# Kernel tuning notes

Measured on AMD Instinct MI355X. Metric: run time of the kernel, lower is better.

## Reference

```python
import jax, jax.numpy as jnp
import numpy as np

H = 16          # num heads
DH = 64         # head dim
D = H * DH      # hidden = 1024


def setup_inputs() -> dict:
    key = jax.random.key(0)
    ks = jax.random.split(key, 9)
    s = 1.0 / np.sqrt(D)
    return {
        "hidden_states": jax.random.normal(ks[0], (4, 2048, D), dtype=jnp.float32),
        "Wq": jax.random.normal(ks[1], (D, D), dtype=jnp.float32) * s,
        "bq": jax.random.normal(ks[2], (D,), dtype=jnp.float32) * 0.02,
        "Wk": jax.random.normal(ks[3], (D, D), dtype=jnp.float32) * s,
        "bk": jax.random.normal(ks[4], (D,), dtype=jnp.float32) * 0.02,
        "Wv": jax.random.normal(ks[5], (D, D), dtype=jnp.float32) * s,
        "bv": jax.random.normal(ks[6], (D,), dtype=jnp.float32) * 0.02,
        "Wo": jax.random.normal(ks[7], (D, D), dtype=jnp.float32) * s,
        "bo": jax.random.normal(ks[8], (D,), dtype=jnp.float32) * 0.02,
    }


def _split_heads(x):  # [B,S,D] -> [B,H,S,DH]
    B, S, _ = x.shape
    return x.reshape(B, S, H, DH).transpose(0, 2, 1, 3)


def reference(hidden_states, Wq, bq, Wk, bk, Wv, bv, Wo, bo):
    # torch Linear: y = x @ W.T + b  (W stored as [out, in])
    q = _split_heads(jnp.einsum('bsd,ed->bse', hidden_states, Wq) + bq)
    k = _split_heads(jnp.einsum('bsd,ed->bse', hidden_states, Wk) + bk)
    v = _split_heads(jnp.einsum('bsd,ed->bse', hidden_states, Wv) + bv)
    scores = jnp.einsum('bhqd,bhkd->bhqk', q, k) / np.sqrt(DH)
    probs = jax.nn.softmax(scores, axis=-1)  # fused softmax+matmul in original
    ctx = jnp.einsum('bhqk,bhkd->bhqd', probs, v)
    B, _, S, _ = ctx.shape
    ctx = ctx.transpose(0, 2, 1, 3).reshape(B, S, D)
    out = jnp.einsum('bsd,ed->bse', ctx, Wo) + bo
    return out  # weights are None (vis=False); dropout rate asserted 0
```

## Files before the change

### kernel.cpp

```cpp
#include <hip/hip_runtime.h>


typedef __bf16 bf16;
typedef __bf16 bf16x8 __attribute__((ext_vector_type(8)));
typedef __bf16 bf16x4 __attribute__((ext_vector_type(4)));
typedef short  short4v __attribute__((ext_vector_type(4)));
typedef float  floatx4 __attribute__((ext_vector_type(4)));

#define NB   4
#define SEQ  2048
#define NH   16
#define DH   64
#define DIM  1024
#define MTOT (NB * SEQ)

#define CEXP 0.18033688f

__device__ __forceinline__ floatx4 zero4() {
    floatx4 z; z[0] = 0.f; z[1] = 0.f; z[2] = 0.f; z[3] = 0.f; return z;
}

__device__ __forceinline__ void load_lds16(const bf16* g, bf16* l) {
    __builtin_amdgcn_global_load_lds(
        (__attribute__((address_space(1))) void*)g,
        (__attribute__((address_space(3))) void*)l,
        16, 0, 0);
}

__device__ __forceinline__ short4v pk4(float a, float b, float c, float d) {
    bf16x4 t; t[0] = (bf16)a; t[1] = (bf16)b; t[2] = (bf16)c; t[3] = (bf16)d;
    return __builtin_bit_cast(short4v, t);
}

__global__ __launch_bounds__(256) void cvt_all(const float* __restrict__ X,
                                               const float* __restrict__ w0,
                                               const float* __restrict__ w1,
                                               const float* __restrict__ w2,
                                               const float* __restrict__ w3,
                                               bf16* __restrict__ Xb,
                                               bf16* __restrict__ Wb) {
    const size_t MD = (size_t)MTOT * DIM;
    const size_t DD = (size_t)DIM * DIM;
    size_t i = ((size_t)blockIdx.x * 256 + threadIdx.x) * 4;
    float4 f; bf16* dst;
    if (i < MD) {
        f = *(const float4*)(X + i);
        dst = Xb + i;
    } else {
        size_t off = i - MD;
        int w = (int)(off >> 20);
        size_t wi = off & (DD - 1);
        const float* ws = (w == 0) ? w0 : (w == 1) ? w1 : (w == 2) ? w2 : w3;
        f = *(const float4*)(ws + wi);
        dst = Wb + off;
    }
    bf16x4 o;
    o[0] = (bf16)f.x; o[1] = (bf16)f.y; o[2] = (bf16)f.z; o[3] = (bf16)f.w;
    *(bf16x4*)dst = o;
}

__global__ __launch_bounds__(256) void gemm_qkv(const bf16* __restrict__ A,
                                                const bf16* __restrict__ W,
                                                const float* __restrict__ bq,
                                                const float* __restrict__ bk,
                                                const float* __restrict__ bv,
                                                bf16* __restrict__ Qo,
                                                bf16* __restrict__ Ko,
                                                bf16* __restrict__ Vt) {
    __shared__ __align__(16) bf16 As[128 * 32];
    __shared__ __align__(16) bf16 Bs[128 * 32];
    __shared__ __align__(16) bf16 Ts[64 * 136];

    const int tid  = threadIdx.x;
    const int wave = tid >> 6, lane = tid & 63;
    const int quad = lane >> 4, l16 = lane & 15;
    const int sel = blockIdx.x >> 3;
    const int nt  = blockIdx.x & 7;
    const int m0 = blockIdx.y * 128, n0 = nt * 128;
    const int wm = (wave & 1) * 64, wn = (wave >> 1) * 64;
    const bf16* Wsel = W + (size_t)(sel * DIM + n0) * DIM;
    const float* bias = (sel == 0) ? bq : (sel == 1) ? bk : bv;
    const float scale = (sel == 0) ? CEXP : 1.0f;

    floatx4 acc[4][4];
#pragma unroll
    for (int mi = 0; mi < 4; mi++)
#pragma unroll
        for (int ni = 0; ni < 4; ni++) acc[mi][ni] = zero4();

    for (int k0 = 0; k0 < DIM; k0 += 32) {
        __syncthreads();
#pragma unroll
        for (int i = 0; i < 2; i++) {
            const int cb = wave * 128 + i * 64;
            const int c  = cb + lane;
            const int row = c >> 2;
            const int kc  = (c & 3) * 8;
            load_lds16(A + (size_t)(m0 + row) * DIM + k0 + kc, &As[cb * 8]);
            load_lds16(Wsel + (size_t)row * DIM + k0 + kc, &Bs[cb * 8]);
        }
        __syncthreads();

        bf16x8 af[4], bfr[4];
#pragma unroll
        for (int mi = 0; mi < 4; mi++)
            af[mi] = *(const bf16x8*)&As[(wm + mi * 16 + l16) * 32 + quad * 8];
#pragma unroll
        for (int ni = 0; ni < 4; ni++)
            bfr[ni] = *(const bf16x8*)&Bs[(wn + ni * 16 + l16) * 32 + quad * 8];
#pragma unroll
        for (int mi = 0; mi < 4; mi++)
#pragma unroll
            for (int ni = 0; ni < 4; ni++)
                acc[mi][ni] = __builtin_amdgcn_mfma_f32_16x16x32_bf16(
                    af[mi], bfr[ni], acc[mi][ni], 0, 0, 0);
    }

    if (sel < 2) {
        bf16* C = (sel == 0) ? Qo : Ko;
#pragma unroll
        for (int mi = 0; mi < 4; mi++) {
            const int rbase = m0 + wm + mi * 16 + quad * 4;
#pragma unroll
            for (int ni = 0; ni < 4; ni++) {
                const int col = n0 + wn + ni * 16 + l16;
                const float bval = bias[col];
#pragma unroll
                for (int i = 0; i < 4; i++)
                    C[(size_t)(rbase + i) * DIM + col] =
                        (bf16)((acc[mi][ni][i] + bval) * scale);
            }
        }
    } else {
        const int b  = blockIdx.y >> 4;
        const int s0 = (blockIdx.y & 15) * 128;
#pragma unroll
        for (int r = 0; r < 2; r++) {
            __syncthreads();
            if ((wave >> 1) == r) {
#pragma unroll
                for (int mi = 0; mi < 4; mi++) {
                    const int m_l = wm + mi * 16 + quad * 4;
#pragma unroll
                    for (int ni = 0; ni < 4; ni++) {
                        const int n_loc = ni * 16 + l16;
                        const float bval = bias[n0 + 64 * r + n_loc];
#pragma unroll
                        for (int i = 0; i < 4; i++)
                            Ts[n_loc * 136 + m_l + i] = (bf16)(acc[mi][ni][i] + bval);
                    }
                }
            }
            __syncthreads();
            const int hh = 2 * nt + r;
            bf16* obase = Vt + ((size_t)(b * NH + hh) * DH) * SEQ + s0;
#pragma unroll
            for (int p = 0; p < 4; p++) {
                const int chunk = p * 256 + tid;
                const int row = chunk >> 4, c0 = (chunk & 15) * 8;
                bf16x8 v = *(const bf16x8*)&Ts[row * 136 + c0];
                *(bf16x8*)(obase + (size_t)row * SEQ + c0) = v;
            }
        }
    }
}

__global__ __launch_bounds__(256) void gemm_out(const bf16* __restrict__ A,
                                                const bf16* __restrict__ W,
                                                const float* __restrict__ bias,
                                                float* __restrict__ C) {
    __shared__ __align__(16) bf16 As[128 * 32];
    __shared__ __align__(16) bf16 Bs[128 * 32];

    const int tid  = threadIdx.x;
    const int wave = tid >> 6, lane = tid & 63;
    const int quad = lane >> 4, l16 = lane & 15;
    const int m0 = blockIdx.y * 128, n0 = blockIdx.x * 128;
    const int wm = (wave & 1) * 64, wn = (wave >> 1) * 64;

    floatx4 acc[4][4];
#pragma unroll
    for (int mi = 0; mi < 4; mi++)
#pragma unroll
        for (int ni = 0; ni < 4; ni++) acc[mi][ni] = zero4();

    for (int k0 = 0; k0 < DIM; k0 += 32) {
        __syncthreads();
#pragma unroll
        for (int i = 0; i < 2; i++) {
            const int cb = wave * 128 + i * 64;
            const int c  = cb + lane;
            const int row = c >> 2;
            const int kc  = (c & 3) * 8;
            load_lds16(A + (size_t)(m0 + row) * DIM + k0 + kc, &As[cb * 8]);
            load_lds16(W + (size_t)(n0 + row) * DIM + k0 + kc, &Bs[cb * 8]);
        }
        __syncthreads();

        bf16x8 af[4], bfr[4];
#pragma unroll
        for (int mi = 0; mi < 4; mi++)
            af[mi] = *(const bf16x8*)&As[(wm + mi * 16 + l16) * 32 + quad * 8];
#pragma unroll
        for (int ni = 0; ni < 4; ni++)
            bfr[ni] = *(const bf16x8*)&Bs[(wn + ni * 16 + l16) * 32 + quad * 8];
#pragma unroll
        for (int mi = 0; mi < 4; mi++)
#pragma unroll
            for (int ni = 0; ni < 4; ni++)
                acc[mi][ni] = __builtin_amdgcn_mfma_f32_16x16x32_bf16(
                    af[mi], bfr[ni], acc[mi][ni], 0, 0, 0);
    }

#pragma unroll
    for (int mi = 0; mi < 4; mi++) {
        const int rbase = m0 + wm + mi * 16 + quad * 4;
#pragma unroll
        for (int ni = 0; ni < 4; ni++) {
            const int col = n0 + wn + ni * 16 + l16;
            const float bval = bias[col];
#pragma unroll
            for (int i = 0; i < 4; i++)
                C[(size_t)(rbase + i) * DIM + col] = acc[mi][ni][i] + bval;
        }
    }
}

__global__ __launch_bounds__(256, 6) void attn_kernel(const bf16* __restrict__ Q,
                                                      const bf16* __restrict__ K,
                                                      const bf16* __restrict__ Vt,
                                                      bf16* __restrict__ Ctx) {
    __shared__ __align__(16) bf16 Ks[2][64 * 64];
    __shared__ __align__(16) bf16 Vs[2][64 * 64];

    const int tid  = threadIdx.x;
    const int wave = tid >> 6, lane = tid & 63;
    const int quad = lane >> 4, l16 = lane & 15;
    const int bh = blockIdx.x >> 5;
    const int qb = blockIdx.x & 31;
    const int b  = bh >> 4, h = bh & 15;

    const size_t base_bh = (size_t)b * SEQ * DIM + (size_t)h * DH;
    const size_t base_v  = (size_t)bh * DH * SEQ;
    const bf16* Kg = K + base_bh;
    const bf16* Vg = Vt + base_v;
    const int qt = qb * 64 + wave * 16;

    const bf16* qp = Q + base_bh + (size_t)(qt + l16) * DIM + quad * 8;
    const bf16x8 aq0 = *(const bf16x8*)qp;
    const bf16x8 aq1 = *(const bf16x8*)(qp + 32);

    const int sc  = wave * 128 + lane;
    const int sr0 = sc >> 3,        sr1 = (sc + 64) >> 3;
    const int sc0 = (sc & 7) ^ (sr0 & 7), sc1 = ((sc + 64) & 7) ^ (sr1 & 7);
    const bf16* kga = Kg + (size_t)sr0 * DIM + sc0 * 8;
    const bf16* kgb = Kg + (size_t)sr1 * DIM + sc1 * 8;
    const bf16* vga = Vg + (size_t)sr0 * SEQ + sc0 * 8;
    const bf16* vgb = Vg + (size_t)sr1 * SEQ + sc1 * 8;

    int koa[4], kob[4], vo[4][4];
#pragma unroll
    for (int t = 0; t < 4; t++) {
        const int krow = t * 16 + l16;
        koa[t] = (krow * 8 + (quad ^ (krow & 7))) * 8;
        kob[t] = (krow * 8 + ((4 + quad) ^ (krow & 7))) * 8;
#pragma unroll
        for (int dt = 0; dt < 4; dt++) {
            const int d = dt * 16 + l16;
            vo[t][dt] = (d * 8 + ((t * 2 + (quad >> 1)) ^ (d & 7))) * 8
                        + (quad & 1) * 4;
        }
    }

    const short4v ones4 = pk4(1.f, 1.f, 1.f, 1.f);

    floatx4 acc[4], accl = zero4();
#pragma unroll
    for (int dt = 0; dt < 4; dt++) acc[dt] = zero4();

    load_lds16(kga, &Ks[0][(wave * 128) * 8]);
    load_lds16(kgb, &Ks[0][(wave * 128 + 64) * 8]);
    load_lds16(vga, &Vs[0][(wave * 128) * 8]);
    load_lds16(vgb, &Vs[0][(wave * 128 + 64) * 8]);

    for (int it = 0; it < SEQ / 64; it++) {
        __syncthreads();
        const int cur = it & 1;
        if (it + 1 < SEQ / 64) {
            const int nxt = cur ^ 1;
            const size_t kvn = (size_t)(it + 1) * 64;
            load_lds16(kga + kvn * DIM, &Ks[nxt][(wave * 128) * 8]);
            load_lds16(kgb + kvn * DIM, &Ks[nxt][(wave * 128 + 64) * 8]);
            load_lds16(vga + kvn, &Vs[nxt][(wave * 128) * 8]);
            load_lds16(vgb + kvn, &Vs[nxt][(wave * 128 + 64) * 8]);
        }

#pragma unroll
        for (int t = 0; t < 4; t++) {
            const bf16x8 kb0 = *(const bf16x8*)&Ks[cur][koa[t]];
            const bf16x8 kb1 = *(const bf16x8*)&Ks[cur][kob[t]];
            short4v vb[4];
#pragma unroll
            for (int dt = 0; dt < 4; dt++)
                vb[dt] = __builtin_bit_cast(short4v,
                    *(const bf16x4*)&Vs[cur][vo[t][dt]]);
            floatx4 z = zero4();
            z = __builtin_amdgcn_mfma_f32_16x16x32_bf16(kb0, aq0, z, 0, 0, 0);
            z = __builtin_amdgcn_mfma_f32_16x16x32_bf16(kb1, aq1, z, 0, 0, 0);
            const short4v p = pk4(__builtin_amdgcn_exp2f(z[0]),
                                  __builtin_amdgcn_exp2f(z[1]),
                                  __builtin_amdgcn_exp2f(z[2]),
                                  __builtin_amdgcn_exp2f(z[3]));
#pragma unroll
            for (int dt = 0; dt < 4; dt++)
                acc[dt] = __builtin_amdgcn_mfma_f32_16x16x16bf16_1k(
                    p, vb[dt], acc[dt], 0, 0, 0);
            accl = __builtin_amdgcn_mfma_f32_16x16x16bf16_1k(
                p, ones4, accl, 0, 0, 0);
        }
    }

    float inv[4];
#pragma unroll
    for (int i = 0; i < 4; i++) inv[i] = 1.0f / accl[i];
    bf16* cp = Ctx + base_bh + (size_t)(qt + quad * 4) * DIM + l16;
#pragma unroll
    for (int i = 0; i < 4; i++)
#pragma unroll
        for (int dt = 0; dt < 4; dt++)
            cp[(size_t)i * DIM + dt * 16] = (bf16)(acc[dt][i] * inv[i]);
}

extern "C" void kernel_launch(void* const* d_in, const int* in_sizes, int n_in,
                              void* d_out, int out_size, void* d_ws, size_t ws_size,
                              hipStream_t stream) {
    const float* X  = (const float*)d_in[0];
    const float* Wq = (const float*)d_in[1];
    const float* bq = (const float*)d_in[2];
    const float* Wk = (const float*)d_in[3];
    const float* bk = (const float*)d_in[4];
    const float* Wv = (const float*)d_in[5];
    const float* bv = (const float*)d_in[6];
    const float* Wo = (const float*)d_in[7];
    const float* bo = (const float*)d_in[8];
    float* out = (float*)d_out;

    const size_t MD = (size_t)MTOT * DIM;
    const size_t DD = (size_t)DIM * DIM;

    bf16* Xb  = (bf16*)d_ws;
    bf16* Qb  = Xb + MD;
    bf16* Kb  = Qb + MD;
    bf16* Vtb = Kb + MD;
    bf16* Wqb = Vtb + MD;
    bf16* Wob = Wqb + 3 * DD;
    if (ws_size < (MD * 4 + DD * 4) * sizeof(bf16)) return;

    cvt_all<<<(int)((MD + 4 * DD) / 4 / 256), 256, 0, stream>>>(
        X, Wq, Wk, Wv, Wo, Xb, Wqb);

    gemm_qkv<<<dim3(24, MTOT / 128), 256, 0, stream>>>(Xb, Wqb, bq, bk, bv,
                                                       Qb, Kb, Vtb);

    attn_kernel<<<NB * NH * (SEQ / 64), 256, 0, stream>>>(Qb, Kb, Vtb, Xb);

    gemm_out<<<dim3(8, MTOT / 128), 256, 0, stream>>>(Xb, Wob, bo, out);
}
```

Baseline: 312.1 us.

## Enlarge attention blocks to 128 queries and halve output GEMM M-tile

The attention kernel now runs 512-thread blocks covering 128 queries (8 waves), so each K/V tile staged in LDS is shared by twice as many queries and every thread issues one load per tile instead of two. The output projection GEMM switches to a 64x128 tile, doubling its grid to 1024 blocks to improve occupancy across CUs. The cost is fewer attention blocks (1024), higher register pressure under the 512-thread launch bound, and less reuse per block in the output GEMM.

```diff
diff --git a/kernel.cpp b/kernel.cpp
--- a/kernel.cpp
+++ b/kernel.cpp
@@ -169,43 +169,47 @@
                                                 const bf16* __restrict__ W,
                                                 const float* __restrict__ bias,
                                                 float* __restrict__ C) {
-    __shared__ __align__(16) bf16 As[128 * 32];
+    __shared__ __align__(16) bf16 As[64 * 32];
     __shared__ __align__(16) bf16 Bs[128 * 32];
 
     const int tid  = threadIdx.x;
     const int wave = tid >> 6, lane = tid & 63;
     const int quad = lane >> 4, l16 = lane & 15;
-    const int m0 = blockIdx.y * 128, n0 = blockIdx.x * 128;
-    const int wm = (wave & 1) * 64, wn = (wave >> 1) * 64;
-
-    floatx4 acc[4][4];
-#pragma unroll
-    for (int mi = 0; mi < 4; mi++)
+    const int m0 = blockIdx.y * 64, n0 = blockIdx.x * 128;
+    const int wm = (wave & 1) * 32, wn = (wave >> 1) * 64;
+
+    floatx4 acc[2][4];
+#pragma unroll
+    for (int mi = 0; mi < 2; mi++)
 #pragma unroll
         for (int ni = 0; ni < 4; ni++) acc[mi][ni] = zero4();
 
     for (int k0 = 0; k0 < DIM; k0 += 32) {
         __syncthreads();
+        {
+            const int c  = tid;
+            const int row = c >> 2, kc = (c & 3) * 8;
+            load_lds16(A + (size_t)(m0 + row) * DIM + k0 + kc,
+                       &As[(wave * 64) * 8]);
+        }
 #pragma unroll
         for (int i = 0; i < 2; i++) {
             const int cb = wave * 128 + i * 64;
             const int c  = cb + lane;
-            const int row = c >> 2;
-            const int kc  = (c & 3) * 8;
-            load_lds16(A + (size_t)(m0 + row) * DIM + k0 + kc, &As[cb * 8]);
+            const int row = c >> 2, kc = (c & 3) * 8;
             load_lds16(W + (size_t)(n0 + row) * DIM + k0 + kc, &Bs[cb * 8]);
         }
         __syncthreads();
 
-        bf16x8 af[4], bfr[4];
-#pragma unroll
-        for (int mi = 0; mi < 4; mi++)
+        bf16x8 af[2], bfr[4];
+#pragma unroll
+        for (int mi = 0; mi < 2; mi++)
             af[mi] = *(const bf16x8*)&As[(wm + mi * 16 + l16) * 32 + quad * 8];
 #pragma unroll
         for (int ni = 0; ni < 4; ni++)
             bfr[ni] = *(const bf16x8*)&Bs[(wn + ni * 16 + l16) * 32 + quad * 8];
 #pragma unroll
-        for (int mi = 0; mi < 4; mi++)
+        for (int mi = 0; mi < 2; mi++)
 #pragma unroll
             for (int ni = 0; ni < 4; ni++)
                 acc[mi][ni] = __builtin_amdgcn_mfma_f32_16x16x32_bf16(
@@ -213,7 +217,7 @@
     }
 
 #pragma unroll
-    for (int mi = 0; mi < 4; mi++) {
+    for (int mi = 0; mi < 2; mi++) {
         const int rbase = m0 + wm + mi * 16 + quad * 4;
 #pragma unroll
         for (int ni = 0; ni < 4; ni++) {
@@ -226,7 +230,7 @@
     }
 }
 
-__global__ __launch_bounds__(256, 6) void attn_kernel(const bf16* __restrict__ Q,
+__global__ __launch_bounds__(512, 8) void attn_kernel(const bf16* __restrict__ Q,
                                                       const bf16* __restrict__ K,
                                                       const bf16* __restrict__ Vt,
                                                       bf16* __restrict__ Ctx) {
@@ -236,27 +240,23 @@
     const int tid  = threadIdx.x;
     const int wave = tid >> 6, lane = tid & 63;
     const int quad = lane >> 4, l16 = lane & 15;
-    const int bh = blockIdx.x >> 5;
-    const int qb = blockIdx.x & 31;
+    const int bh = blockIdx.x >> 4;
+    const int qb = blockIdx.x & 15;
     const int b  = bh >> 4, h = bh & 15;
 
     const size_t base_bh = (size_t)b * SEQ * DIM + (size_t)h * DH;
     const size_t base_v  = (size_t)bh * DH * SEQ;
-    const bf16* Kg = K + base_bh;
-    const bf16* Vg = Vt + base_v;
-    const int qt = qb * 64 + wave * 16;
+    const int qt = qb * 128 + wave * 16;
 
     const bf16* qp = Q + base_bh + (size_t)(qt + l16) * DIM + quad * 8;
     const bf16x8 aq0 = *(const bf16x8*)qp;
     const bf16x8 aq1 = *(const bf16x8*)(qp + 32);
 
-    const int sc  = wave * 128 + lane;
-    const int sr0 = sc >> 3,        sr1 = (sc + 64) >> 3;
-    const int sc0 = (sc & 7) ^ (sr0 & 7), sc1 = ((sc + 64) & 7) ^ (sr1 & 7);
-    const bf16* kga = Kg + (size_t)sr0 * DIM + sc0 * 8;
-    const bf16* kgb = Kg + (size_t)sr1 * DIM + sc1 * 8;
-    const bf16* vga = Vg + (size_t)sr0 * SEQ + sc0 * 8;
-    const bf16* vgb = Vg + (size_t)sr1 * SEQ + sc1 * 8;
+    const int sr = tid >> 3;
+    const int sc8 = (tid & 7) ^ (sr & 7);
+    const bf16* kga = K + base_bh + (size_t)sr * DIM + sc8 * 8;
+    const bf16* vga = Vt + base_v + (size_t)sr * SEQ + sc8 * 8;
+    const int ldst = (wave * 64) * 8;
 
     int koa[4], kob[4], vo[4][4];
 #pragma unroll
@@ -278,10 +278,8 @@
 #pragma unroll
     for (int dt = 0; dt < 4; dt++) acc[dt] = zero4();
 
-    load_lds16(kga, &Ks[0][(wave * 128) * 8]);
-    load_lds16(kgb, &Ks[0][(wave * 128 + 64) * 8]);
-    load_lds16(vga, &Vs[0][(wave * 128) * 8]);
-    load_lds16(vgb, &Vs[0][(wave * 128 + 64) * 8]);
+    load_lds16(kga, &Ks[0][ldst]);
+    load_lds16(vga, &Vs[0][ldst]);
 
     for (int it = 0; it < SEQ / 64; it++) {
         __syncthreads();
@@ -289,10 +287,8 @@
         if (it + 1 < SEQ / 64) {
             const int nxt = cur ^ 1;
             const size_t kvn = (size_t)(it + 1) * 64;
-            load_lds16(kga + kvn * DIM, &Ks[nxt][(wave * 128) * 8]);
-            load_lds16(kgb + kvn * DIM, &Ks[nxt][(wave * 128 + 64) * 8]);
-            load_lds16(vga + kvn, &Vs[nxt][(wave * 128) * 8]);
-            load_lds16(vgb + kvn, &Vs[nxt][(wave * 128 + 64) * 8]);
+            load_lds16(kga + kvn * DIM, &Ks[nxt][ldst]);
+            load_lds16(vga + kvn, &Vs[nxt][ldst]);
         }
 
 #pragma unroll
@@ -362,7 +358,7 @@
     gemm_qkv<<<dim3(24, MTOT / 128), 256, 0, stream>>>(Xb, Wqb, bq, bk, bv,
                                                        Qb, Kb, Vtb);
 
-    attn_kernel<<<NB * NH * (SEQ / 64), 256, 0, stream>>>(Qb, Kb, Vtb, Xb);
-
-    gemm_out<<<dim3(8, MTOT / 128), 256, 0, stream>>>(Xb, Wob, bo, out);
-}
+    attn_kernel<<<NB * NH * (SEQ / 128), 512, 0, stream>>>(Qb, Kb, Vtb, Xb);
+
+    gemm_out<<<dim3(8, MTOT / 64), 256, 0, stream>>>(Xb, Wob, bo, out);
+}
```

Measured after the change: 311.5 us. No clear change (-0.2%).

## Process two query tiles per wave in attention to reuse K/V LDS fragments

Applied to the files above, without the earlier changes.

Each attention block now covers 128 queries instead of 64, with each wave handling two 16-row query tiles that share the same K and V fragments read from LDS. This halves the K/V global-to-LDS traffic and the LDS reads per query, and halves the grid size. In exchange, register use per thread roughly doubles for accumulators and Q fragments, so the launch-bounds occupancy hint is lowered from 6 to 4 blocks per CU, and there are fewer blocks to spread across CUs.

```diff
diff --git a/kernel.cpp b/kernel.cpp
--- a/kernel.cpp
+++ b/kernel.cpp
@@ -226,7 +226,7 @@
     }
 }
 
-__global__ __launch_bounds__(256, 6) void attn_kernel(const bf16* __restrict__ Q,
+__global__ __launch_bounds__(256, 4) void attn_kernel(const bf16* __restrict__ Q,
                                                       const bf16* __restrict__ K,
                                                       const bf16* __restrict__ Vt,
                                                       bf16* __restrict__ Ctx) {
@@ -236,27 +236,30 @@
     const int tid  = threadIdx.x;
     const int wave = tid >> 6, lane = tid & 63;
     const int quad = lane >> 4, l16 = lane & 15;
-    const int bh = blockIdx.x >> 5;
-    const int qb = blockIdx.x & 31;
+    const int bh = blockIdx.x >> 4;
+    const int qb = blockIdx.x & 15;
     const int b  = bh >> 4, h = bh & 15;
 
     const size_t base_bh = (size_t)b * SEQ * DIM + (size_t)h * DH;
     const size_t base_v  = (size_t)bh * DH * SEQ;
-    const bf16* Kg = K + base_bh;
-    const bf16* Vg = Vt + base_v;
-    const int qt = qb * 64 + wave * 16;
-
-    const bf16* qp = Q + base_bh + (size_t)(qt + l16) * DIM + quad * 8;
-    const bf16x8 aq0 = *(const bf16x8*)qp;
-    const bf16x8 aq1 = *(const bf16x8*)(qp + 32);
+    const int qt = qb * 128 + wave * 32;
+
+    bf16x8 aq[2][2];
+#pragma unroll
+    for (int m = 0; m < 2; m++) {
+        const bf16* qp = Q + base_bh + (size_t)(qt + m * 16 + l16) * DIM + quad * 8;
+        aq[m][0] = *(const bf16x8*)qp;
+        aq[m][1] = *(const bf16x8*)(qp + 32);
+    }
 
     const int sc  = wave * 128 + lane;
     const int sr0 = sc >> 3,        sr1 = (sc + 64) >> 3;
     const int sc0 = (sc & 7) ^ (sr0 & 7), sc1 = ((sc + 64) & 7) ^ (sr1 & 7);
-    const bf16* kga = Kg + (size_t)sr0 * DIM + sc0 * 8;
-    const bf16* kgb = Kg + (size_t)sr1 * DIM + sc1 * 8;
-    const bf16* vga = Vg + (size_t)sr0 * SEQ + sc0 * 8;
-    const bf16* vgb = Vg + (size_t)sr1 * SEQ + sc1 * 8;
+    const bf16* kga = K + base_bh + (size_t)sr0 * DIM + sc0 * 8;
+    const bf16* kgb = K + base_bh + (size_t)sr1 * DIM + sc1 * 8;
+    const bf16* vga = Vt + base_v + (size_t)sr0 * SEQ + sc0 * 8;
+    const bf16* vgb = Vt + base_v + (size_t)sr1 * SEQ + sc1 * 8;
+    const int ldsa = (wave * 128) * 8, ldsb = (wave * 128 + 64) * 8;
 
     int koa[4], kob[4], vo[4][4];
 #pragma unroll
@@ -274,14 +277,18 @@
 
     const short4v ones4 = pk4(1.f, 1.f, 1.f, 1.f);
 
-    floatx4 acc[4], accl = zero4();
-#pragma unroll
-    for (int dt = 0; dt < 4; dt++) acc[dt] = zero4();
-
-    load_lds16(kga, &Ks[0][(wave * 128) * 8]);
-    load_lds16(kgb, &Ks[0][(wave * 128 + 64) * 8]);
-    load_lds16(vga, &Vs[0][(wave * 128) * 8]);
-    load_lds16(vgb, &Vs[0][(wave * 128 + 64) * 8]);
+    floatx4 acc[2][4], accl[2];
+#pragma unroll
+    for (int m = 0; m < 2; m++) {
+        accl[m] = zero4();
+#pragma unroll
+        for (int dt = 0; dt < 4; dt++) acc[m][dt] = zero4();
+    }
+
+    load_lds16(kga, &Ks[0][ldsa]);
+    load_lds16(kgb, &Ks[0][ldsb]);
+    load_lds16(vga, &Vs[0][ldsa]);
+    load_lds16(vgb, &Vs[0][ldsb]);
 
     for (int it = 0; it < SEQ / 64; it++) {
         __syncthreads();
@@ -289,10 +296,10 @@
         if (it + 1 < SEQ / 64) {
             const int nxt = cur ^ 1;
             const size_t kvn = (size_t)(it + 1) * 64;
-            load_lds16(kga + kvn * DIM, &Ks[nxt][(wave * 128) * 8]);
-            load_lds16(kgb + kvn * DIM, &Ks[nxt][(wave * 128 + 64) * 8]);
-            load_lds16(vga + kvn, &Vs[nxt][(wave * 128) * 8]);
-            load_lds16(vgb + kvn, &Vs[nxt][(wave * 128 + 64) * 8]);
+            load_lds16(kga + kvn * DIM, &Ks[nxt][ldsa]);
+            load_lds16(kgb + kvn * DIM, &Ks[nxt][ldsb]);
+            load_lds16(vga + kvn, &Vs[nxt][ldsa]);
+            load_lds16(vgb + kvn, &Vs[nxt][ldsb]);
         }
 
 #pragma unroll
@@ -304,31 +311,37 @@
             for (int dt = 0; dt < 4; dt++)
                 vb[dt] = __builtin_bit_cast(short4v,
                     *(const bf16x4*)&Vs[cur][vo[t][dt]]);
-            floatx4 z = zero4();
-            z = __builtin_amdgcn_mfma_f32_16x16x32_bf16(kb0, aq0, z, 0, 0, 0);
-            z = __builtin_amdgcn_mfma_f32_16x16x32_bf16(kb1, aq1, z, 0, 0, 0);
-            const short4v p = pk4(__builtin_amdgcn_exp2f(z[0]),
-                                  __builtin_amdgcn_exp2f(z[1]),
-                                  __builtin_amdgcn_exp2f(z[2]),
-                                  __builtin_amdgcn_exp2f(z[3]));
+#pragma unroll
+            for (int m = 0; m < 2; m++) {
+                floatx4 z = zero4();
+                z = __builtin_amdgcn_mfma_f32_16x16x32_bf16(kb0, aq[m][0], z, 0, 0, 0);
+                z = __builtin_amdgcn_mfma_f32_16x16x32_bf16(kb1, aq[m][1], z, 0, 0, 0);
+                const short4v p = pk4(__builtin_amdgcn_exp2f(z[0]),
+                                      __builtin_amdgcn_exp2f(z[1]),
+                                      __builtin_amdgcn_exp2f(z[2]),
+                                      __builtin_amdgcn_exp2f(z[3]));
+#pragma unroll
+                for (int dt = 0; dt < 4; dt++)
+                    acc[m][dt] = __builtin_amdgcn_mfma_f32_16x16x16bf16_1k(
+                        p, vb[dt], acc[m][dt], 0, 0, 0);
+                accl[m] = __builtin_amdgcn_mfma_f32_16x16x16bf16_1k(
+                    p, ones4, accl[m], 0, 0, 0);
+            }
+        }
+    }
+
+#pragma unroll
+    for (int m = 0; m < 2; m++) {
+        float inv[4];
+#pragma unroll
+        for (int i = 0; i < 4; i++) inv[i] = 1.0f / accl[m][i];
+        bf16* cp = Ctx + base_bh + (size_t)(qt + m * 16 + quad * 4) * DIM + l16;
+#pragma unroll
+        for (int i = 0; i < 4; i++)
 #pragma unroll
             for (int dt = 0; dt < 4; dt++)
-                acc[dt] = __builtin_amdgcn_mfma_f32_16x16x16bf16_1k(
-                    p, vb[dt], acc[dt], 0, 0, 0);
-            accl = __builtin_amdgcn_mfma_f32_16x16x16bf16_1k(
-                p, ones4, accl, 0, 0, 0);
-        }
-    }
-
-    float inv[4];
-#pragma unroll
-    for (int i = 0; i < 4; i++) inv[i] = 1.0f / accl[i];
-    bf16* cp = Ctx + base_bh + (size_t)(qt + quad * 4) * DIM + l16;
-#pragma unroll
-    for (int i = 0; i < 4; i++)
-#pragma unroll
-        for (int dt = 0; dt < 4; dt++)
-            cp[(size_t)i * DIM + dt * 16] = (bf16)(acc[dt][i] * inv[i]);
+                cp[(size_t)i * DIM + dt * 16] = (bf16)(acc[m][dt][i] * inv[i]);
+    }
 }
 
 extern "C" void kernel_launch(void* const* d_in, const int* in_sizes, int n_in,
@@ -362,7 +375,7 @@
     gemm_qkv<<<dim3(24, MTOT / 128), 256, 0, stream>>>(Xb, Wqb, bq, bk, bv,
                                                        Qb, Kb, Vtb);
 
-    attn_kernel<<<NB * NH * (SEQ / 64), 256, 0, stream>>>(Qb, Kb, Vtb, Xb);
+    attn_kernel<<<NB * NH * (SEQ / 128), 256, 0, stream>>>(Qb, Kb, Vtb, Xb);
 
     gemm_out<<<dim3(8, MTOT / 128), 256, 0, stream>>>(Xb, Wob, bo, out);
 }
```

Measured after the change: 298.2 us. -4.4%, faster.
